# Kernel tuning notes

Hardware: AMD Instinct MI355X
Metric: run time of the kernel (lower is better)

## Reference

```python
import jax, jax.numpy as jnp
import numpy as np

C = 256
CQK = C // 8  # 32

def setup_inputs() -> dict:
    key = jax.random.key(0)
    ks = jax.random.split(key, 8)
    B, H, W = 8, 64, 64
    x = jax.random.normal(ks[0], (B, C, H, W), dtype=jnp.float32)
    y = jax.random.normal(ks[1], (B, C, H, W), dtype=jnp.float32)
    s = 1.0 / np.sqrt(C)
    Wq = jax.random.normal(ks[2], (CQK, C), dtype=jnp.float32) * s
    bq = jnp.zeros((CQK,), dtype=jnp.float32)
    Wk = jax.random.normal(ks[3], (CQK, C), dtype=jnp.float32) * s
    bk = jnp.zeros((CQK,), dtype=jnp.float32)
    Wv = jax.random.normal(ks[4], (C, C), dtype=jnp.float32) * s
    bv = jnp.zeros((C,), dtype=jnp.float32)
    return {"x": x, "y": y, "Wq": Wq, "bq": bq, "Wk": Wk, "bk": bk, "Wv": Wv, "bv": bv}

def reference(x, y, Wq, bq, Wk, bk, Wv, bv):
    B, Cc, H, W = x.shape
    HW = H * W
    xf = x.reshape(B, Cc, HW)  # [B,C,HW]
    yf = y.reshape(B, Cc, HW)
    # 1x1 convs == per-pixel linear projections
    Q = jnp.einsum('oc,bcn->bno', Wq, xf) + bq          # [B,HW,CQK]
    K = jnp.einsum('oc,bcn->bon', Wk, yf) + bk[:, None]  # [B,CQK,HW]
    V = jnp.einsum('oc,bcn->bon', Wv, yf) + bv[:, None]  # [B,C,HW]
    attn = jax.nn.softmax(jnp.einsum('bnd,bdm->bnm', Q, K), axis=-1)  # [B,HW,HW]
    out = jnp.einsum('bcm,bnm->bcn', V, attn)  # V @ attn^T -> [B,C,HW]
    return out.reshape(B, Cc, H, W)
```

## Files before the change

### kernel.cpp

```cpp
#include <hip/hip_runtime.h>

typedef unsigned short u16;
typedef _Float16 f16;
typedef __attribute__((ext_vector_type(8))) short v8s;
typedef __attribute__((ext_vector_type(4))) short v4s;
typedef __attribute__((ext_vector_type(8))) f16   v8h;
typedef __attribute__((ext_vector_type(4))) float v4f;
typedef __attribute__((ext_vector_type(16))) float v16f;
typedef __attribute__((ext_vector_type(4))) unsigned v4u;

#define NB   8
#define NC   256
#define DQK  32
#define NPIX 4096

__device__ __forceinline__ u16 f2bf(float f) {
  unsigned u = __builtin_bit_cast(unsigned, f);
  u += 0x7FFFu + ((u >> 16) & 1u);
  return (u16)(u >> 16);
}
__device__ __forceinline__ u16 f2h(float f) {
  return __builtin_bit_cast(u16, (f16)f);
}
__device__ __forceinline__ unsigned cvt_pk_bf16(float lo, float hi) {
  unsigned r;
  asm("v_cvt_pk_bf16_f32 %0, %1, %2" : "=v"(r) : "v"(lo), "v"(hi));
  return r;
}
__device__ __forceinline__ float fast_exp2(float x) {
  float r;
  asm("v_exp_f32 %0, %1" : "=v"(r) : "v"(x));
  return r;
}

__global__ __launch_bounds__(256)
void convert_w(const float* __restrict__ Wq, const float* __restrict__ Wk,
               const float* __restrict__ Wv,
               u16* __restrict__ Whq, u16* __restrict__ Whk, u16* __restrict__ Whv) {
  int i = blockIdx.x * 256 + threadIdx.x;
  if (i < 8192)       Whq[i]         = f2h(Wq[i]);
  else if (i < 16384) Whk[i - 8192]  = f2h(Wk[i - 8192]);
  else                Whv[i - 16384] = f2h(Wv[i - 16384]);
}

__global__ __launch_bounds__(256)
void xpose(const float* __restrict__ x, const float* __restrict__ y,
           u16* __restrict__ xt, u16* __restrict__ yt) {
  const float* __restrict__ src = blockIdx.y ? y : x;
  u16* __restrict__ dst         = blockIdx.y ? yt : xt;
  const int bid = blockIdx.x;
  const int b  = bid >> 8;
  const int c0 = ((bid >> 6) & 3) * 64;
  const int n0 = (bid & 63) * 64;
  __shared__ u16 T[64][66];
  const int t = threadIdx.x, nl = t & 63, cq = t >> 6;
  const float* __restrict__ s = src + ((size_t)b << 20) + (size_t)c0 * NPIX + n0;
#pragma unroll
  for (int i = 0; i < 16; ++i) {
    int c = cq * 16 + i;
    T[c][nl] = f2h(s[(size_t)c * NPIX + nl]);
  }
  __syncthreads();
  u16* __restrict__ d = dst + ((size_t)b << 20) + (size_t)n0 * NC + c0;
#pragma unroll
  for (int i = 0; i < 2; ++i) {
    int nr = (t >> 3) + 32 * i, c8 = (t & 7) * 8;
    v8s v;
#pragma unroll
    for (int j = 0; j < 8; ++j) v[j] = (short)T[c8 + j][nr];
    *(v8s*)(d + (size_t)nr * NC + c8) = v;
  }
}

__global__ __launch_bounds__(256)
void proj_mfma(const u16* __restrict__ xt, const u16* __restrict__ yt,
               const u16* __restrict__ Whq, const float* __restrict__ bq,
               const u16* __restrict__ Whk, const float* __restrict__ bk,
               const u16* __restrict__ Whv, const float* __restrict__ bv,
               u16* __restrict__ Qb, u16* __restrict__ Kb, u16* __restrict__ Vt) {
  const int tid = threadIdx.x, w = tid >> 6, lane = tid & 63;
  const int lr = lane & 15, quad = lane >> 4;
  const int b = blockIdx.x & 7;
  const int n0 = (blockIdx.x >> 3) * 64;
  const int n = n0 + w * 16 + lr;
  const size_t bn = ((size_t)b << 12) + n;

  v8h xb[8], yb[8];
  const u16* xp = xt + bn * NC + quad * 8;
  const u16* yp = yt + bn * NC + quad * 8;
#pragma unroll
  for (int t = 0; t < 8; ++t) {
    xb[t] = *(const v8h*)(xp + 32 * t);
    yb[t] = *(const v8h*)(yp + 32 * t);
  }

#pragma unroll
  for (int ot = 0; ot < 2; ++ot) {
    v4f aq = {0.f, 0.f, 0.f, 0.f}, ak = {0.f, 0.f, 0.f, 0.f};
#pragma unroll
    for (int t = 0; t < 8; ++t) {
      v8h wq = *(const v8h*)(Whq + (ot * 16 + lr) * 256 + quad * 8 + 32 * t);
      v8h wk = *(const v8h*)(Whk + (ot * 16 + lr) * 256 + quad * 8 + 32 * t);
      aq = __builtin_amdgcn_mfma_f32_16x16x32_f16(wq, xb[t], aq, 0, 0, 0);
      ak = __builtin_amdgcn_mfma_f32_16x16x32_f16(wk, yb[t], ak, 0, 0, 0);
    }
    v4f bqv = *(const v4f*)(bq + ot * 16 + quad * 4);
    v4f bkv = *(const v4f*)(bk + ot * 16 + quad * 4);
    v4s q4, k4;
#pragma unroll
    for (int r = 0; r < 4; ++r) {
      q4[r] = (short)f2h(aq[r] + bqv[r]);
      k4[r] = (short)f2h(ak[r] + bkv[r]);
    }
    *(v4s*)(Qb + bn * DQK + ot * 16 + quad * 4) = q4;
    *(v4s*)(Kb + bn * DQK + ot * 16 + quad * 4) = k4;
  }

  for (int vt = 0; vt < 16; ++vt) {
    v4f av = {0.f, 0.f, 0.f, 0.f};
#pragma unroll
    for (int t = 0; t < 8; ++t) {
      v8h wv = *(const v8h*)(Whv + (vt * 16 + lr) * 256 + quad * 8 + 32 * t);
      av = __builtin_amdgcn_mfma_f32_16x16x32_f16(wv, yb[t], av, 0, 0, 0);
    }
#pragma unroll
    for (int r = 0; r < 4; ++r) {
      int o = vt * 16 + quad * 4 + r;
      size_t off = ((((size_t)b * 64 + (n >> 6)) * 32 + (o >> 5) * 4 + ((n >> 4) & 3)) * 64
                    + ((n >> 3) & 1) * 32 + (o & 31)) * 8 + (n & 7);
      Vt[off] = f2bf(av[r] + bv[o]);
    }
  }
}

#define L2E  1.44269504f
#define SHFT -48.0f

#define PACK_TILE(S, PBLO, PBHI)                                              \
  {                                                                           \
    float e0  = fast_exp2(fmaf(S[0],  L2E, SHFT));                            \
    float e1  = fast_exp2(fmaf(S[1],  L2E, SHFT));                            \
    float e2  = fast_exp2(fmaf(S[2],  L2E, SHFT));                            \
    float e3  = fast_exp2(fmaf(S[3],  L2E, SHFT));                            \
    float e4  = fast_exp2(fmaf(S[4],  L2E, SHFT));                            \
    float e5  = fast_exp2(fmaf(S[5],  L2E, SHFT));                            \
    float e6  = fast_exp2(fmaf(S[6],  L2E, SHFT));                            \
    float e7  = fast_exp2(fmaf(S[7],  L2E, SHFT));                            \
    float e8  = fast_exp2(fmaf(S[8],  L2E, SHFT));                            \
    float e9  = fast_exp2(fmaf(S[9],  L2E, SHFT));                            \
    float e10 = fast_exp2(fmaf(S[10], L2E, SHFT));                            \
    float e11 = fast_exp2(fmaf(S[11], L2E, SHFT));                            \
    float e12 = fast_exp2(fmaf(S[12], L2E, SHFT));                            \
    float e13 = fast_exp2(fmaf(S[13], L2E, SHFT));                            \
    float e14 = fast_exp2(fmaf(S[14], L2E, SHFT));                            \
    float e15 = fast_exp2(fmaf(S[15], L2E, SHFT));                            \
    lsum += (((e0 + e1) + (e2 + e3)) + ((e4 + e5) + (e6 + e7)))               \
          + (((e8 + e9) + (e10 + e11)) + ((e12 + e13) + (e14 + e15)));        \
    unsigned u00 = cvt_pk_bf16(e0,  e1),  u01 = cvt_pk_bf16(e2,  e3);         \
    unsigned u10 = cvt_pk_bf16(e4,  e5),  u11 = cvt_pk_bf16(e6,  e7);         \
    unsigned u20 = cvt_pk_bf16(e8,  e9),  u21 = cvt_pk_bf16(e10, e11);        \
    unsigned u30 = cvt_pk_bf16(e12, e13), u31 = cvt_pk_bf16(e14, e15);        \
    asm("v_permlane32_swap_b32 %0, %1" : "+v"(u00), "+v"(u10));               \
    asm("v_permlane32_swap_b32 %0, %1" : "+v"(u01), "+v"(u11));               \
    asm("v_permlane32_swap_b32 %0, %1" : "+v"(u20), "+v"(u30));               \
    asm("v_permlane32_swap_b32 %0, %1" : "+v"(u21), "+v"(u31));               \
    PBLO = __builtin_bit_cast(v8s, (v4u){u00, u01, u10, u11});                \
    PBHI = __builtin_bit_cast(v8s, (v4u){u20, u21, u30, u31});                \
  }

__global__ __launch_bounds__(256, 1)
void attn_kernel(const u16* __restrict__ Qb, const u16* __restrict__ Kb,
                 const u16* __restrict__ Vt, float* __restrict__ out) {
  __shared__ __attribute__((aligned(16))) u16 Vb[2][32][64][8];

  const int tid  = threadIdx.x;
  const int w    = tid >> 6;
  const int lane = tid & 63;
  const int l31  = lane & 31;
  const int h    = lane >> 5;

  const int b  = blockIdx.x & 7;
  const int q0 = (blockIdx.x >> 3) << 7;
  const int qw = q0 + w * 32;

  const u16* Qp = Qb + ((size_t)b * NPIX + qw + l31) * DQK + h * 8;
  const v8h qf0 = *(const v8h*)(Qp);
  const v8h qf1 = *(const v8h*)(Qp + 16);

  const u16* Kp = Kb + ((size_t)b * NPIX + l31) * DQK + h * 8;

  const u16* Vg = Vt + ((size_t)b << 20) + (size_t)lane * 8;

  v16f acc[8];
#pragma unroll
  for (int i = 0; i < 8; ++i) acc[i] = (v16f){};
  float lsum = 0.f;
  const v16f vz = (v16f){};

#pragma unroll
  for (int j = 0; j < 8; ++j) {
    const int f = w * 8 + j;
    __builtin_amdgcn_global_load_lds(
        (const __attribute__((address_space(1))) unsigned*)(Vg + (size_t)f * 512),
        (__attribute__((address_space(3))) unsigned*)(&Vb[0][f][0][0]), 16, 0, 0);
  }
  v8h kc0 = *(const v8h*)(Kp);
  v8h kc1 = *(const v8h*)(Kp + 16);
  v8h kc2 = *(const v8h*)(Kp + 1024);
  v8h kc3 = *(const v8h*)(Kp + 1040);
  v8h kn0 = kc0, kn1 = kc1, kn2 = kc2, kn3 = kc3;

  v8s pB0, pB1, pB2, pB3;
  {
    v16f sA = __builtin_amdgcn_mfma_f32_32x32x16_f16(kc0, qf0, vz, 0, 0, 0);
    sA = __builtin_amdgcn_mfma_f32_32x32x16_f16(kc1, qf1, sA, 0, 0, 0);
    v16f sB = __builtin_amdgcn_mfma_f32_32x32x16_f16(kc2, qf0, vz, 0, 0, 0);
    sB = __builtin_amdgcn_mfma_f32_32x32x16_f16(kc3, qf1, sB, 0, 0, 0);
    PACK_TILE(sA, pB0, pB1);
    PACK_TILE(sB, pB2, pB3);
  }
  {
    const u16* kp1 = Kp + 2048;
    kc0 = *(const v8h*)(kp1);
    kc1 = *(const v8h*)(kp1 + 16);
    kc2 = *(const v8h*)(kp1 + 1024);
    kc3 = *(const v8h*)(kp1 + 1040);
  }

#pragma unroll 1
  for (int it = 0; it < 64; ++it) {
    const int p = it & 1;
    __builtin_amdgcn_sched_barrier(0);
    if (it < 63) {
      asm volatile("s_waitcnt vmcnt(4)" ::: "memory");
    } else {
      asm volatile("s_waitcnt vmcnt(0)" ::: "memory");
    }
    __builtin_amdgcn_s_barrier();
    __builtin_amdgcn_sched_barrier(0);

    if (it < 63) {
#pragma unroll
      for (int j = 0; j < 8; ++j) {
        const int f = w * 8 + j;
        __builtin_amdgcn_global_load_lds(
            (const __attribute__((address_space(1))) unsigned*)(Vg + ((size_t)(it + 1) * 32 + f) * 512),
            (__attribute__((address_space(3))) unsigned*)(&Vb[p ^ 1][f][0][0]), 16, 0, 0);
      }
    }

#pragma unroll
    for (int ct = 0; ct < 8; ++ct) {
      v8s vf0 = *(const v8s*)(&Vb[p][ct * 4 + 0][lane][0]);
      v8s vf1 = *(const v8s*)(&Vb[p][ct * 4 + 1][lane][0]);
      v8s vf2 = *(const v8s*)(&Vb[p][ct * 4 + 2][lane][0]);
      v8s vf3 = *(const v8s*)(&Vb[p][ct * 4 + 3][lane][0]);
      acc[ct] = __builtin_amdgcn_mfma_f32_32x32x16_bf16(vf0, pB0, acc[ct], 0, 0, 0);
      acc[ct] = __builtin_amdgcn_mfma_f32_32x32x16_bf16(vf1, pB1, acc[ct], 0, 0, 0);
      acc[ct] = __builtin_amdgcn_mfma_f32_32x32x16_bf16(vf2, pB2, acc[ct], 0, 0, 0);
      acc[ct] = __builtin_amdgcn_mfma_f32_32x32x16_bf16(vf3, pB3, acc[ct], 0, 0, 0);
    }

    if (it < 63) {
      v16f sA = __builtin_amdgcn_mfma_f32_32x32x16_f16(kc0, qf0, vz, 0, 0, 0);
      sA = __builtin_amdgcn_mfma_f32_32x32x16_f16(kc1, qf1, sA, 0, 0, 0);
      v16f sB = __builtin_amdgcn_mfma_f32_32x32x16_f16(kc2, qf0, vz, 0, 0, 0);
      sB = __builtin_amdgcn_mfma_f32_32x32x16_f16(kc3, qf1, sB, 0, 0, 0);
      if (it < 62) {
        const u16* kp2 = Kp + (size_t)(it + 2) * 2048;
        kn0 = *(const v8h*)(kp2);
        kn1 = *(const v8h*)(kp2 + 16);
        kn2 = *(const v8h*)(kp2 + 1024);
        kn3 = *(const v8h*)(kp2 + 1040);
      }
      PACK_TILE(sA, pB0, pB1);
      PACK_TILE(sB, pB2, pB3);
      kc0 = kn0; kc1 = kn1; kc2 = kn2; kc3 = kn3;
    }
  }

  lsum += __shfl_xor(lsum, 32);
  const float linv = 1.0f / lsum;

  float* op = out + (size_t)b * NC * NPIX + q0 + w * 32 + l31;
#pragma unroll
  for (int ct = 0; ct < 8; ++ct)
#pragma unroll
    for (int r = 0; r < 16; ++r) {
      const int ch = ct * 32 + (r & 3) + ((r >> 2) << 3) + (h << 2);
      op[(size_t)ch * NPIX] = acc[ct][r] * linv;
    }
}

extern "C" void kernel_launch(void* const* d_in, const int* in_sizes, int n_in,
                              void* d_out, int out_size, void* d_ws, size_t ws_size,
                              hipStream_t stream) {
  const float* x  = (const float*)d_in[0];
  const float* y  = (const float*)d_in[1];
  const float* Wq = (const float*)d_in[2];
  const float* bq = (const float*)d_in[3];
  const float* Wk = (const float*)d_in[4];
  const float* bk = (const float*)d_in[5];
  const float* Wv = (const float*)d_in[6];
  const float* bv = (const float*)d_in[7];
  float* out = (float*)d_out;

  u16* Qb  = (u16*)d_ws;
  u16* Kb  = Qb + (size_t)NB * NPIX * DQK;
  u16* Vt  = Kb + (size_t)NB * NPIX * DQK;
  u16* xt  = Vt + (size_t)NB * NC * NPIX;
  u16* yt  = xt + (size_t)NB * NPIX * NC;
  u16* Whq = yt + (size_t)NB * NPIX * NC;
  u16* Whk = Whq + 32 * 256;
  u16* Whv = Whk + 32 * 256;

  hipLaunchKernelGGL(convert_w, dim3(320), dim3(256), 0, stream, Wq, Wk, Wv, Whq, Whk, Whv);
  hipLaunchKernelGGL(xpose, dim3(2048, 2), dim3(256), 0, stream, x, y, xt, yt);
  hipLaunchKernelGGL(proj_mfma, dim3(512), dim3(256), 0, stream,
                     xt, yt, Whq, bq, Whk, bk, Whv, bv, Qb, Kb, Vt);
  hipLaunchKernelGGL(attn_kernel, dim3(256), dim3(256), 0, stream, Qb, Kb, Vt, out);
}
```

Before: 268.0 us.

## Split attention key range across two wave groups and reduce partials via LDS

The attention block grows from 256 to 512 threads. Two groups of four waves each process half of the key/value sequence with their own double-buffered V staging, and the partial accumulators and row sums are then combined through shared memory before the output is written. The aim is twice as many waves per CU, with more latency hiding and MFMA utilisation, using a grid of only 256 blocks. Costs are extra LDS for the wider buffer plus a reduction pass. MFMA sections also get s_setprio raised so they are favoured while loads are in flight.

```diff
diff --git a/kernel.cpp b/kernel.cpp
--- a/kernel.cpp
+++ b/kernel.cpp
@@ -168,28 +168,32 @@
     PBHI = __builtin_bit_cast(v8s, (v4u){u20, u21, u30, u31});                \
   }
 
-__global__ __launch_bounds__(256, 1)
+__global__ __launch_bounds__(512, 2)
 void attn_kernel(const u16* __restrict__ Qb, const u16* __restrict__ Kb,
                  const u16* __restrict__ Vt, float* __restrict__ out) {
-  __shared__ __attribute__((aligned(16))) u16 Vb[2][32][64][8];
+  __shared__ __attribute__((aligned(16))) u16 Vb[4][32][64][8];
+  __shared__ float Ls2[4][32];
 
   const int tid  = threadIdx.x;
   const int w    = tid >> 6;
   const int lane = tid & 63;
   const int l31  = lane & 31;
-  const int h    = lane >> 5;
+  const int wq   = w & 3;
+  const int g    = w >> 2;
+  const int bufbase = g * 2;
 
   const int b  = blockIdx.x & 7;
   const int q0 = (blockIdx.x >> 3) << 7;
-  const int qw = q0 + w * 32;
-
+  const int qw = q0 + wq * 32;
+
+  const int h = lane >> 5;
   const u16* Qp = Qb + ((size_t)b * NPIX + qw + l31) * DQK + h * 8;
   const v8h qf0 = *(const v8h*)(Qp);
   const v8h qf1 = *(const v8h*)(Qp + 16);
 
-  const u16* Kp = Kb + ((size_t)b * NPIX + l31) * DQK + h * 8;
-
-  const u16* Vg = Vt + ((size_t)b << 20) + (size_t)lane * 8;
+  const u16* Kp = Kb + ((size_t)b * NPIX + l31) * DQK + h * 8 + (size_t)g * 32 * 2048;
+
+  const u16* Vg = Vt + ((size_t)b << 20) + (size_t)lane * 8 + (size_t)g * 32 * 16384;
 
   v16f acc[8];
 #pragma unroll
@@ -199,10 +203,10 @@
 
 #pragma unroll
   for (int j = 0; j < 8; ++j) {
-    const int f = w * 8 + j;
+    const int f = wq * 8 + j;
     __builtin_amdgcn_global_load_lds(
         (const __attribute__((address_space(1))) unsigned*)(Vg + (size_t)f * 512),
-        (__attribute__((address_space(3))) unsigned*)(&Vb[0][f][0][0]), 16, 0, 0);
+        (__attribute__((address_space(3))) unsigned*)(&Vb[bufbase][f][0][0]), 16, 0, 0);
   }
   v8h kc0 = *(const v8h*)(Kp);
   v8h kc1 = *(const v8h*)(Kp + 16);
@@ -228,10 +232,10 @@
   }
 
 #pragma unroll 1
-  for (int it = 0; it < 64; ++it) {
-    const int p = it & 1;
+  for (int it = 0; it < 32; ++it) {
+    const int pp = it & 1;
     __builtin_amdgcn_sched_barrier(0);
-    if (it < 63) {
+    if (it < 31) {
       asm volatile("s_waitcnt vmcnt(4)" ::: "memory");
     } else {
       asm volatile("s_waitcnt vmcnt(0)" ::: "memory");
@@ -239,34 +243,36 @@
     __builtin_amdgcn_s_barrier();
     __builtin_amdgcn_sched_barrier(0);
 
-    if (it < 63) {
+    if (it < 31) {
 #pragma unroll
       for (int j = 0; j < 8; ++j) {
-        const int f = w * 8 + j;
+        const int f = wq * 8 + j;
         __builtin_amdgcn_global_load_lds(
             (const __attribute__((address_space(1))) unsigned*)(Vg + ((size_t)(it + 1) * 32 + f) * 512),
-            (__attribute__((address_space(3))) unsigned*)(&Vb[p ^ 1][f][0][0]), 16, 0, 0);
-      }
-    }
-
+            (__attribute__((address_space(3))) unsigned*)(&Vb[bufbase + (pp ^ 1)][f][0][0]), 16, 0, 0);
+      }
+    }
+
+    __builtin_amdgcn_s_setprio(1);
 #pragma unroll
     for (int ct = 0; ct < 8; ++ct) {
-      v8s vf0 = *(const v8s*)(&Vb[p][ct * 4 + 0][lane][0]);
-      v8s vf1 = *(const v8s*)(&Vb[p][ct * 4 + 1][lane][0]);
-      v8s vf2 = *(const v8s*)(&Vb[p][ct * 4 + 2][lane][0]);
-      v8s vf3 = *(const v8s*)(&Vb[p][ct * 4 + 3][lane][0]);
+      v8s vf0 = *(const v8s*)(&Vb[bufbase + pp][ct * 4 + 0][lane][0]);
+      v8s vf1 = *(const v8s*)(&Vb[bufbase + pp][ct * 4 + 1][lane][0]);
+      v8s vf2 = *(const v8s*)(&Vb[bufbase + pp][ct * 4 + 2][lane][0]);
+      v8s vf3 = *(const v8s*)(&Vb[bufbase + pp][ct * 4 + 3][lane][0]);
       acc[ct] = __builtin_amdgcn_mfma_f32_32x32x16_bf16(vf0, pB0, acc[ct], 0, 0, 0);
       acc[ct] = __builtin_amdgcn_mfma_f32_32x32x16_bf16(vf1, pB1, acc[ct], 0, 0, 0);
       acc[ct] = __builtin_amdgcn_mfma_f32_32x32x16_bf16(vf2, pB2, acc[ct], 0, 0, 0);
       acc[ct] = __builtin_amdgcn_mfma_f32_32x32x16_bf16(vf3, pB3, acc[ct], 0, 0, 0);
     }
-
-    if (it < 63) {
+    __builtin_amdgcn_s_setprio(0);
+
+    if (it < 31) {
       v16f sA = __builtin_amdgcn_mfma_f32_32x32x16_f16(kc0, qf0, vz, 0, 0, 0);
       sA = __builtin_amdgcn_mfma_f32_32x32x16_f16(kc1, qf1, sA, 0, 0, 0);
       v16f sB = __builtin_amdgcn_mfma_f32_32x32x16_f16(kc2, qf0, vz, 0, 0, 0);
       sB = __builtin_amdgcn_mfma_f32_32x32x16_f16(kc3, qf1, sB, 0, 0, 0);
-      if (it < 62) {
+      if (it < 30) {
         const u16* kp2 = Kp + (size_t)(it + 2) * 2048;
         kn0 = *(const v8h*)(kp2);
         kn1 = *(const v8h*)(kp2 + 16);
@@ -280,16 +286,42 @@
   }
 
   lsum += __shfl_xor(lsum, 32);
-  const float linv = 1.0f / lsum;
-
-  float* op = out + (size_t)b * NC * NPIX + q0 + w * 32 + l31;
-#pragma unroll
-  for (int ct = 0; ct < 8; ++ct)
-#pragma unroll
-    for (int r = 0; r < 16; ++r) {
-      const int ch = ct * 32 + (r & 3) + ((r >> 2) << 3) + (h << 2);
-      op[(size_t)ch * NPIX] = acc[ct][r] * linv;
-    }
+
+  __syncthreads();
+  float* Cb = (float*)&Vb[0][0][0][0];
+  if (w >= 4) {
+    const int w4 = w - 4;
+#pragma unroll
+    for (int ct = 0; ct < 8; ++ct)
+#pragma unroll
+      for (int k = 0; k < 4; ++k) {
+        v4f c = {acc[ct][k * 4 + 0], acc[ct][k * 4 + 1],
+                 acc[ct][k * 4 + 2], acc[ct][k * 4 + 3]};
+        *(v4f*)(Cb + (((w4 * 32 + ct * 4 + k) * 64 + lane) << 2)) = c;
+      }
+    if (lane < 32) Ls2[w4][l31] = lsum;
+  }
+  __syncthreads();
+  if (w < 4) {
+    const float linv = 1.0f / (lsum + Ls2[w][l31]);
+#pragma unroll
+    for (int ct = 0; ct < 8; ++ct)
+#pragma unroll
+      for (int k = 0; k < 4; ++k) {
+        v4f c = *(const v4f*)(Cb + (((w * 32 + ct * 4 + k) * 64 + lane) << 2));
+        acc[ct][k * 4 + 0] += c[0]; acc[ct][k * 4 + 1] += c[1];
+        acc[ct][k * 4 + 2] += c[2]; acc[ct][k * 4 + 3] += c[3];
+      }
+
+    float* op = out + (size_t)b * NC * NPIX + q0 + wq * 32 + l31;
+#pragma unroll
+    for (int ct = 0; ct < 8; ++ct)
+#pragma unroll
+      for (int r = 0; r < 16; ++r) {
+        const int ch = ct * 32 + (r & 3) + ((r >> 2) << 3) + (h << 2);
+        op[(size_t)ch * NPIX] = acc[ct][r] * linv;
+      }
+  }
 }
 
 extern "C" void kernel_launch(void* const* d_in, const int* in_sizes, int n_in,
@@ -318,5 +350,5 @@
   hipLaunchKernelGGL(xpose, dim3(2048, 2), dim3(256), 0, stream, x, y, xt, yt);
   hipLaunchKernelGGL(proj_mfma, dim3(512), dim3(256), 0, stream,
                      xt, yt, Whq, bq, Whk, bk, Whv, bv, Qb, Kb, Vt);
-  hipLaunchKernelGGL(attn_kernel, dim3(256), dim3(256), 0, stream, Qb, Kb, Vt, out);
-}
+  hipLaunchKernelGGL(attn_kernel, dim3(256), dim3(512), 0, stream, Qb, Kb, Vt, out);
+}
```

Result: faster. 250.6 us (-6.5%).
